# Optimization experiments

Measured on AMD Instinct MI355X. Metric: run time of the kernel, lower is better.

Reference implementation:

```python
import jax, jax.numpy as jnp
import numpy as np

D_MODEL = 1024
NUM_HEADS = 16
D_K = D_MODEL // NUM_HEADS
B, S = 4, 2048


def setup_inputs() -> dict:
    key = jax.random.key(0)
    ks = jax.random.split(key, 12)
    Q = jax.random.normal(ks[0], (B, S, D_MODEL), dtype=jnp.float32)
    K = jax.random.normal(ks[1], (B, S, D_MODEL), dtype=jnp.float32)
    V = jax.random.normal(ks[2], (B, S, D_MODEL), dtype=jnp.float32)
    # causal mask: 1 where attention allowed, 0 where blocked
    mask = jnp.tril(jnp.ones((S, S), dtype=jnp.int32))[None, None, :, :]
    sc = 1.0 / np.sqrt(D_MODEL)
    Wq = jax.random.normal(ks[3], (D_MODEL, D_MODEL), dtype=jnp.float32) * sc
    Wk = jax.random.normal(ks[4], (D_MODEL, D_MODEL), dtype=jnp.float32) * sc
    Wv = jax.random.normal(ks[5], (D_MODEL, D_MODEL), dtype=jnp.float32) * sc
    Wo = jax.random.normal(ks[6], (D_MODEL, D_MODEL), dtype=jnp.float32) * sc
    bq = jnp.zeros((D_MODEL,), dtype=jnp.float32)
    bk = jnp.zeros((D_MODEL,), dtype=jnp.float32)
    bv = jnp.zeros((D_MODEL,), dtype=jnp.float32)
    bo = jnp.zeros((D_MODEL,), dtype=jnp.float32)
    return {"Q": Q, "K": K, "V": V, "mask": mask,
            "Wq": Wq, "bq": bq, "Wk": Wk, "bk": bk,
            "Wv": Wv, "bv": bv, "Wo": Wo, "bo": bo}


def reference(Q, K, V, mask, Wq, bq, Wk, bk, Wv, bv, Wo, bo):
    b = Q.shape[0]
    # projections (torch Linear: x @ W.T + b; here W stored as [in, out])
    q = Q @ Wq + bq
    k = K @ Wk + bk
    v = V @ Wv + bv
    # [B, S, D] -> [B, H, S, d_k]
    def split_heads(x):
        return x.reshape(b, -1, NUM_HEADS, D_K).transpose(0, 2, 1, 3)
    q, k, v = split_heads(q), split_heads(k), split_heads(v)
    scores = jnp.einsum('bhqd,bhkd->bhqk', q, k) / jnp.sqrt(jnp.float32(D_K))
    scores = jnp.where(mask == 0, -jnp.inf, scores)
    attn = jax.nn.softmax(scores, axis=-1)
    out = jnp.einsum('bhqk,bhkd->bhqd', attn, v)  # [B, H, S, d_k]
    out = out.transpose(0, 2, 1, 3).reshape(b, -1, NUM_HEADS * D_K)
    return out @ Wo + bo
```

## Files before the change

### kernel.cpp

```cpp
#include <hip/hip_runtime.h>

typedef __bf16 bf16_t;
typedef __bf16 bf16x8 __attribute__((ext_vector_type(8)));
typedef __bf16 bf16x4 __attribute__((ext_vector_type(4)));
typedef float  floatx4 __attribute__((ext_vector_type(4)));

#define D_MODEL 1024
#define S_LEN   2048
#define NHEAD   16
#define DK      64
#define BATCH   4
#define MROWS   (BATCH * S_LEN)
#define QSCALE  0.18033688011112042f

__device__ __forceinline__ void load_lds16(const void* gsrc, void* ldst) {
  __builtin_amdgcn_global_load_lds(
      (const __attribute__((address_space(1))) void*)gsrc,
      (__attribute__((address_space(3))) void*)ldst, 16, 0, 0);
}

__device__ __forceinline__ unsigned pack_bf16(float a, float b) {
  union { bf16_t h[2]; unsigned u; } t;
  t.h[0] = (bf16_t)a; t.h[1] = (bf16_t)b;
  return t.u;
}

__device__ __forceinline__ float bperm_f(int addr, float v) {
  union { float f; int i; } in, out;
  in.f = v;
  out.i = __builtin_amdgcn_ds_bpermute(addr, in.i);
  return out.f;
}

__device__ __forceinline__ void barrier_mem() {
  asm volatile("" ::: "memory");
  __builtin_amdgcn_s_barrier();
  asm volatile("" ::: "memory");
}

__global__ __launch_bounds__(256)
void convert_a_kernel(const float* __restrict__ Q, const float* __restrict__ K,
                      const float* __restrict__ V, bf16_t* __restrict__ Abf)
{
  const int z = blockIdx.y;
  const float* src = z == 0 ? Q : (z == 1 ? K : V);
  bf16_t* dst = Abf + ((size_t)z << 23);
  const size_t off = ((size_t)blockIdx.x * 256 + threadIdx.x) * 8;
  floatx4 a = *(const floatx4*)&src[off];
  floatx4 b = *(const floatx4*)&src[off + 4];
  bf16x8 o;
  o[0] = (bf16_t)a[0]; o[1] = (bf16_t)a[1];
  o[2] = (bf16_t)a[2]; o[3] = (bf16_t)a[3];
  o[4] = (bf16_t)b[0]; o[5] = (bf16_t)b[1];
  o[6] = (bf16_t)b[2]; o[7] = (bf16_t)b[3];
  *(bf16x8*)&dst[off] = o;
}

__global__ __launch_bounds__(256)
void transpose_w_kernel(const float* __restrict__ W0, const float* __restrict__ W1,
                        const float* __restrict__ W2, const float* __restrict__ W3,
                        bf16_t* __restrict__ T0, bf16_t* __restrict__ T1,
                        bf16_t* __restrict__ T2, bf16_t* __restrict__ T3)
{
  const int z = blockIdx.z;
  const float* W = z == 0 ? W0 : (z == 1 ? W1 : (z == 2 ? W2 : W3));
  bf16_t* Wt     = z == 0 ? T0 : (z == 1 ? T1 : (z == 2 ? T2 : T3));

  __shared__ float tile[64][65];
  const int x0 = blockIdx.x * 64;
  const int y0 = blockIdx.y * 64;
  const int tid = threadIdx.x;
  const int r = tid >> 4;
  const int c = (tid & 15) << 2;
#pragma unroll
  for (int p = 0; p < 4; p++) {
    floatx4 v = *(const floatx4*)&W[(size_t)(y0 + p * 16 + r) * D_MODEL + x0 + c];
    tile[p * 16 + r][c + 0] = v[0];
    tile[p * 16 + r][c + 1] = v[1];
    tile[p * 16 + r][c + 2] = v[2];
    tile[p * 16 + r][c + 3] = v[3];
  }
  __syncthreads();
#pragma unroll
  for (int p = 0; p < 4; p++) {
    int row = p * 16 + r;
    bf16x4 o;
    o[0] = (bf16_t)tile[c + 0][row];
    o[1] = (bf16_t)tile[c + 1][row];
    o[2] = (bf16_t)tile[c + 2][row];
    o[3] = (bf16_t)tile[c + 3][row];
    *(bf16x4*)&Wt[(size_t)(x0 + row) * D_MODEL + y0 + c] = o;
  }
}

__global__ __launch_bounds__(512, 2)
void qkv8_kernel(const bf16_t* __restrict__ Abf, const bf16_t* __restrict__ Wcat,
                 const float* __restrict__ bq, const float* __restrict__ bk,
                 const float* __restrict__ bv,
                 bf16_t* __restrict__ qo, bf16_t* __restrict__ ko,
                 bf16_t* __restrict__ vo)
{
  __shared__ bf16_t lds[2][3][128 * 64];

  const int orig = blockIdx.x;
  const int L = (orig & 7) * 96 + (orig >> 3);
  const int bm = L / 12, bn = L % 12;
  const int m0 = bm << 7;
  const int n0 = bn << 8;
  const int z  = n0 >> 10;
  const bf16_t* A = Abf + ((size_t)z << 23);

  const int tid = threadIdx.x;
  const int wid = tid >> 6, lane = tid & 63;
  const int l15 = lane & 15, quad = lane >> 4;
  const int wm = wid >> 2, wn = wid & 3;

  floatx4 acc[4][4] = {};
  bf16x8 Af[2][2], Bf[2][2];

  auto stage_half = [&](int buf, int half, int kt) {
    const bf16_t* src = half == 0
        ? (A + (size_t)m0 * D_MODEL)
        : (Wcat + (size_t)(n0 + ((half - 1) << 7)) * D_MODEL);
    const int k0 = (kt & 15) << 6;
    bf16_t* dst = &lds[buf][half][0];
#pragma unroll
    for (int p = 0; p < 2; p++) {
      const int slot = (p << 9) + tid;
      const int row = slot >> 3;
      const int c = (slot & 7) ^ (row & 7);
      load_lds16(&src[(size_t)row * D_MODEL + k0 + (c << 3)],
                 &dst[(size_t)((p << 9) + (wid << 6)) << 3]);
    }
  };

#define PHASE(BUF, MH, NH, RDA, RDB, DOST, SBUF, SHALF, SKT, VMW)              \
  {                                                                            \
    if (RDA) {                                                                 \
      _Pragma("unroll") for (int mi = 0; mi < 2; mi++) {                       \
        const int row = (wm << 6) + (((MH) * 2 + mi) << 4) + l15;              \
        _Pragma("unroll") for (int ks = 0; ks < 2; ks++) {                     \
          const int ck = (ks << 2) + quad;                                     \
          Af[mi][ks] = *(const bf16x8*)&lds[BUF][0]                            \
              [(row << 6) + ((ck ^ (row & 7)) << 3)];                          \
        }                                                                      \
      }                                                                        \
    }                                                                          \
    if (RDB) {                                                                 \
      _Pragma("unroll") for (int ni = 0; ni < 2; ni++) {                       \
        const int row = ((wn & 1) << 6) + (((NH) * 2 + ni) << 4) + l15;        \
        _Pragma("unroll") for (int ks = 0; ks < 2; ks++) {                     \
          const int ck = (ks << 2) + quad;                                     \
          Bf[ni][ks] = *(const bf16x8*)&lds[BUF][1 + (wn >> 1)]                \
              [(row << 6) + ((ck ^ (row & 7)) << 3)];                          \
        }                                                                      \
      }                                                                        \
    }                                                                          \
    if (DOST) stage_half(SBUF, SHALF, SKT);                                    \
    barrier_mem();                                                             \
    __builtin_amdgcn_s_setprio(1);                                             \
    _Pragma("unroll") for (int mi = 0; mi < 2; mi++)                           \
      _Pragma("unroll") for (int ni = 0; ni < 2; ni++)                         \
        _Pragma("unroll") for (int ks = 0; ks < 2; ks++)                       \
          acc[(MH) * 2 + mi][(NH) * 2 + ni] =                                  \
              __builtin_amdgcn_mfma_f32_16x16x32_bf16(                         \
                  Af[mi][ks], Bf[ni][ks],                                      \
                  acc[(MH) * 2 + mi][(NH) * 2 + ni], 0, 0, 0);                 \
    __builtin_amdgcn_s_setprio(0);                                             \
    if (VMW) asm volatile("s_waitcnt vmcnt(2)" ::: "memory");                  \
    barrier_mem();                                                             \
  }

  stage_half(0, 0, 0);
  stage_half(0, 1, 0);
  stage_half(0, 2, 0);
  stage_half(1, 0, 1);
  asm volatile("s_waitcnt vmcnt(2)" ::: "memory");
  barrier_mem();

  for (int it = 0; it < 8; it++) {
    const int tv  = 2 * it + 1;
    const int tu2 = 2 * it + 2;
    const int tv2 = 2 * it + 3;
    PHASE(0, 0, 0, 1, 1, 1, 1, 1, tv,  0)
    PHASE(0, 0, 1, 0, 1, 1, 1, 2, tv,  0)
    PHASE(0, 1, 1, 1, 0, 0, 0, 0, 0,   0)
    PHASE(0, 1, 0, 0, 1, 1, 0, 0, tu2, 1)
    PHASE(1, 0, 0, 1, 1, 1, 0, 1, tu2, 0)
    PHASE(1, 0, 1, 0, 1, 1, 0, 2, tu2, 0)
    PHASE(1, 1, 1, 1, 0, 0, 0, 0, 0,   0)
    PHASE(1, 1, 0, 0, 1, 1, 1, 0, tv2, 1)
  }
  asm volatile("s_waitcnt vmcnt(0)" ::: "memory");

#undef PHASE

  const float* bias = z == 0 ? bq : (z == 1 ? bk : bv);
  bf16_t* outp      = z == 0 ? qo : (z == 1 ? ko : vo);
  const float scl   = (z == 0) ? QSCALE : 1.0f;
#pragma unroll
  for (int mi = 0; mi < 4; mi++) {
#pragma unroll
    for (int ni = 0; ni < 4; ni++) {
      const int nn = (n0 + (wn << 6) + (ni << 4) + l15) & (D_MODEL - 1);
      const float bvv = bias[nn];
      const int h = nn >> 6, d = nn & 63;
#pragma unroll
      for (int r = 0; r < 4; r++) {
        const int m = m0 + (wm << 6) + (mi << 4) + quad * 4 + r;
        const int b = m >> 11, srow = m & (S_LEN - 1);
        float v = (acc[mi][ni][r] + bvv) * scl;
        if (z < 2) {
          outp[((((size_t)(b * NHEAD + h) << 11) + srow) << 6) + d] = (bf16_t)v;
        } else {
          outp[((((size_t)(b * NHEAD + h) << 6) + d) << 11) + srow] = (bf16_t)v;
        }
      }
    }
  }
}

__global__ __launch_bounds__(256, 3)
void qkv_legacy_kernel(const float* __restrict__ Qi, const float* __restrict__ Ki,
                       const float* __restrict__ Vi, const bf16_t* __restrict__ Wcat,
                       const float* __restrict__ bq, const float* __restrict__ bk,
                       const float* __restrict__ bv,
                       bf16_t* __restrict__ qo, bf16_t* __restrict__ ko,
                       bf16_t* __restrict__ vo)
{
  __shared__ float  Asf[128 * 32];
  __shared__ bf16_t Bs[128 * 32];

  const int L = blockIdx.x + 24 * blockIdx.y;
  const int j = (L >> 3) & 7;
  const int s = ((L >> 6) << 3) | (L & 7);
  const int z = s >> 6;
  const int n0g = (((z << 3) | j)) << 7;
  const int m0 = (s & 63) << 7;

  const float* A = z == 0 ? Qi : (z == 1 ? Ki : Vi);

  const int tid = threadIdx.x;
  const int lane = tid & 63;
  const int w = tid >> 6;
  const int l15 = lane & 15;
  const int quad = lane >> 4;
  const int wy = (w >> 1) << 6;
  const int wx = (w & 1) << 6;
  const int w64 = w << 6;

  floatx4 acc[4][4];
#pragma unroll
  for (int i = 0; i < 4; i++)
#pragma unroll
    for (int jj = 0; jj < 4; jj++)
#pragma unroll
      for (int r = 0; r < 4; r++) acc[i][jj][r] = 0.0f;

  for (int kt = 0; kt < 32; kt++) {
    const int k0 = kt << 5;
    __syncthreads();
#pragma unroll
    for (int p = 0; p < 2; p++) {
      int slot = p * 256 + w64 + lane;
      int row = slot >> 2;
      int kc = (slot & 3) ^ (row & 3);
      load_lds16(&Wcat[(size_t)(n0g + row) * D_MODEL + k0 + (kc << 3)],
                 &Bs[(size_t)(p * 256 + w64) << 3]);
    }
#pragma unroll
    for (int p = 0; p < 4; p++) {
      int sbase = (w << 8) + (p << 6);
      int slot = sbase + lane;
      int row = slot >> 3;
      int ca = (slot & 7) ^ (row & 7);
      load_lds16(&A[(size_t)(m0 + row) * D_MODEL + k0 + (ca << 2)],
                 &Asf[(size_t)sbase << 2]);
    }
    __syncthreads();

    bf16x8 af[4], bfv[4];
#pragma unroll
    for (int mi = 0; mi < 4; mi++) {
      const int m = wy + mi * 16 + l15;
      const int e = m & 7;
      floatx4 f0 = *(const floatx4*)&Asf[(m << 5) + ((((quad << 1))     ^ e) << 2)];
      floatx4 f1 = *(const floatx4*)&Asf[(m << 5) + ((((quad << 1) | 1) ^ e) << 2)];
      bf16x8 o;
      o[0] = (bf16_t)f0[0]; o[1] = (bf16_t)f0[1];
      o[2] = (bf16_t)f0[2]; o[3] = (bf16_t)f0[3];
      o[4] = (bf16_t)f1[0]; o[5] = (bf16_t)f1[1];
      o[6] = (bf16_t)f1[2]; o[7] = (bf16_t)f1[3];
      af[mi] = o;
    }
#pragma unroll
    for (int ni = 0; ni < 4; ni++) {
      int n = wx + ni * 16 + l15;
      bfv[ni] = *(const bf16x8*)&Bs[n * 32 + ((quad ^ (n & 3)) << 3)];
    }
#pragma unroll
    for (int mi = 0; mi < 4; mi++)
#pragma unroll
      for (int ni = 0; ni < 4; ni++)
        acc[mi][ni] = __builtin_amdgcn_mfma_f32_16x16x32_bf16(
            af[mi], bfv[ni], acc[mi][ni], 0, 0, 0);
  }

  const float* bias = z == 0 ? bq : (z == 1 ? bk : bv);
  bf16_t* outp      = z == 0 ? qo : (z == 1 ? ko : vo);
  const float scl   = (z == 0) ? QSCALE : 1.0f;
#pragma unroll
  for (int mi = 0; mi < 4; mi++) {
#pragma unroll
    for (int ni = 0; ni < 4; ni++) {
      const int nn = (n0g + wx + ni * 16 + l15) & (D_MODEL - 1);
      const float bvv = bias[nn];
      const int h = nn >> 6, d = nn & 63;
#pragma unroll
      for (int r = 0; r < 4; r++) {
        const int m = m0 + wy + mi * 16 + quad * 4 + r;
        const int b = m >> 11, srow = m & (S_LEN - 1);
        float v = (acc[mi][ni][r] + bvv) * scl;
        if (z < 2) {
          outp[((((size_t)(b * NHEAD + h) << 11) + srow) << 6) + d] = (bf16_t)v;
        } else {
          outp[((((size_t)(b * NHEAD + h) << 6) + d) << 11) + srow] = (bf16_t)v;
        }
      }
    }
  }
}

__global__ __launch_bounds__(256)
void out_gemm_kernel(const bf16_t* __restrict__ A, const bf16_t* __restrict__ Wt,
                     const float* __restrict__ bias, float* __restrict__ out)
{
  __shared__ bf16_t As[128 * 32];
  __shared__ bf16_t Bs[128 * 32];
  const int L = blockIdx.x + 8 * blockIdx.y;
  const int n0 = (((L >> 3) & 7)) << 7;
  const int m0 = ((((L >> 6) << 3) | (L & 7))) << 7;
  const int tid = threadIdx.x;
  const int lane = tid & 63;
  const int w = tid >> 6;
  const int l15 = lane & 15;
  const int quad = lane >> 4;
  const int wy = (w >> 1) << 6;
  const int wx = (w & 1) << 6;
  const int w64 = w << 6;

  floatx4 acc[4][4];
#pragma unroll
  for (int i = 0; i < 4; i++)
#pragma unroll
    for (int jj = 0; jj < 4; jj++)
#pragma unroll
      for (int r = 0; r < 4; r++) acc[i][jj][r] = 0.0f;

  for (int kt = 0; kt < 32; kt++) {
    const int k0 = kt << 5;
    __syncthreads();
#pragma unroll
    for (int p = 0; p < 2; p++) {
      int slot = p * 256 + w64 + lane;
      int row = slot >> 2;
      int kc = (slot & 3) ^ (row & 3);
      load_lds16(&A[(size_t)(m0 + row) * D_MODEL + k0 + (kc << 3)],
                 &As[(size_t)(p * 256 + w64) << 3]);
      load_lds16(&Wt[(size_t)(n0 + row) * D_MODEL + k0 + (kc << 3)],
                 &Bs[(size_t)(p * 256 + w64) << 3]);
    }
    __syncthreads();

    bf16x8 af[4], bfv[4];
#pragma unroll
    for (int mi = 0; mi < 4; mi++) {
      int m = wy + mi * 16 + l15;
      af[mi] = *(const bf16x8*)&As[m * 32 + ((quad ^ (m & 3)) << 3)];
    }
#pragma unroll
    for (int ni = 0; ni < 4; ni++) {
      int n = wx + ni * 16 + l15;
      bfv[ni] = *(const bf16x8*)&Bs[n * 32 + ((quad ^ (n & 3)) << 3)];
    }
#pragma unroll
    for (int mi = 0; mi < 4; mi++)
#pragma unroll
      for (int ni = 0; ni < 4; ni++)
        acc[mi][ni] = __builtin_amdgcn_mfma_f32_16x16x32_bf16(
            af[mi], bfv[ni], acc[mi][ni], 0, 0, 0);
  }

#pragma unroll
  for (int mi = 0; mi < 4; mi++) {
#pragma unroll
    for (int ni = 0; ni < 4; ni++) {
      const int nbase = n0 + wx + ni * 16 + l15;
      const float bv = bias[nbase];
#pragma unroll
      for (int r = 0; r < 4; r++) {
        const int m = m0 + wy + mi * 16 + quad * 4 + r;
        out[((size_t)m << 10) + nbase] = acc[mi][ni][r] + bv;
      }
    }
  }
}

__global__ __launch_bounds__(256, 4)
void attn_kernel(const bf16_t* __restrict__ qp, const bf16_t* __restrict__ kp,
                 const bf16_t* __restrict__ vtp, bf16_t* __restrict__ ob)
{
  __shared__ bf16_t Kt0[64 * 64];
  __shared__ bf16_t Kt1[64 * 64];
  __shared__ bf16_t Vt0[64 * 64];
  __shared__ bf16_t Vt1[64 * 64];

  const int lin = blockIdx.x + (blockIdx.y << 4);
  const int pair = (lin >> 3) & 15;
  const int bh = (lin & 7) | ((lin >> 7) << 3);
  const int tid = threadIdx.x;
  const int w = tid >> 6;
  const int lane = tid & 63;
  const int l15 = lane & 15;
  const int quad = lane >> 4;

  const bf16_t* Qh = qp + ((size_t)bh << 17);
  const bf16_t* Kh = kp + ((size_t)bh << 17);
  const bf16_t* Vh = vtp + ((size_t)bh << 17);
  const int b = bh >> 4, h = bh & 15;

  auto stage = [&](int k0s, bf16_t* dK, bf16_t* dV) {
#pragma unroll
    for (int p = 0; p < 2; p++) {
      const int sbase = (w << 7) + (p << 6);
      const int slot = sbase + lane;
      const int row = slot >> 3;
      const int c = (slot & 7) ^ (row & 7);
      load_lds16(&Kh[((size_t)(k0s + row) << 6) + (c << 3)], &dK[sbase << 3]);
      load_lds16(&Vh[((size_t)row << 11) + k0s + (c << 3)], &dV[sbase << 3]);
    }
  };

  int par = 0;

  auto phase = [&](int qt, bool prefetch_next_phase) {
    const int q0 = qt << 6;
    const int qbase = q0 + (w << 4);
    const int nkb = qt + 1;

    bf16x8 qf[2];
#pragma unroll
    for (int ks = 0; ks < 2; ks++)
      qf[ks] = *(const bf16x8*)&Qh[(size_t)(qbase + l15) * DK +
                                   ks * 32 + (quad << 3)];

    floatx4 acc_o[4];
    float m_i = -1e30f, l_i = 0.0f;
#pragma unroll
    for (int nd = 0; nd < 4; nd++)
#pragma unroll
      for (int r = 0; r < 4; r++) acc_o[nd][r] = 0.0f;

    for (int kb = 0; kb < nkb; kb++) {
      const int k0 = kb << 6;
      __syncthreads();

      const bf16_t* cK = par ? Kt1 : Kt0;
      const bf16_t* cV = par ? Vt1 : Vt0;
      bf16_t* nK = par ? Kt0 : Kt1;
      bf16_t* nV = par ? Vt0 : Vt1;

      if (kb + 1 < nkb)             stage((kb + 1) << 6, nK, nV);
      else if (prefetch_next_phase) stage(0, nK, nV);

      bf16x8 bk[2][4];
#pragma unroll
      for (int ks = 0; ks < 2; ks++)
#pragma unroll
        for (int ni = 0; ni < 4; ni++) {
          const int row = ni * 16 + l15;
          const int cp = ((ks << 2) + quad) ^ (row & 7);
          bk[ks][ni] = *(const bf16x8*)&cK[(row << 6) + (cp << 3)];
        }

      floatx4 st[4];
#pragma unroll
      for (int ni = 0; ni < 4; ni++)
#pragma unroll
        for (int r = 0; r < 4; r++) st[ni][r] = 0.0f;
      __builtin_amdgcn_s_setprio(1);
#pragma unroll
      for (int ks = 0; ks < 2; ks++)
#pragma unroll
        for (int ni = 0; ni < 4; ni++)
          st[ni] = __builtin_amdgcn_mfma_f32_16x16x32_bf16(
              bk[ks][ni], qf[ks], st[ni], 0, 0, 0);
      __builtin_amdgcn_s_setprio(0);

      if (k0 + 63 > qbase) {
        const int qrow = qbase + l15;
#pragma unroll
        for (int ni = 0; ni < 4; ni++) {
          const int keyb = k0 + ni * 16 + quad * 4;
#pragma unroll
          for (int r = 0; r < 4; r++)
            if (keyb + r > qrow) st[ni][r] = -1e30f;
        }
      }

      float v = st[0][0];
#pragma unroll
      for (int ni = 0; ni < 4; ni++)
#pragma unroll
        for (int r = 0; r < 4; r++) v = fmaxf(v, st[ni][r]);
      v = fmaxf(v, __shfl_xor(v, 16));
      v = fmaxf(v, __shfl_xor(v, 32));

      if (!__all(v <= m_i + 5.0f)) {
        const float mn = fmaxf(m_i, v);
        const float alpha = __builtin_amdgcn_exp2f(m_i - mn);
        m_i = mn;
        l_i *= alpha;
#pragma unroll
        for (int r = 0; r < 4; r++) {
          float ab = bperm_f((quad * 4 + r) << 2, alpha);
#pragma unroll
          for (int nd = 0; nd < 4; nd++) acc_o[nd][r] *= ab;
        }
      }

      unsigned pd[4][2];
      float ssum = 0.0f;
#pragma unroll
      for (int c = 0; c < 4; c++)
#pragma unroll
        for (int hh = 0; hh < 2; hh++) {
          float p0 = __builtin_amdgcn_exp2f(st[c][2 * hh]     - m_i);
          float p1 = __builtin_amdgcn_exp2f(st[c][2 * hh + 1] - m_i);
          ssum += p0 + p1;
          pd[c][hh] = pack_bf16(p0, p1);
        }
      ssum += __shfl_xor(ssum, 16);
      ssum += __shfl_xor(ssum, 32);
      l_i += ssum;

      union AV { unsigned u[4]; bf16x8 v; };
      AV av[2];
#pragma unroll
      for (int ks = 0; ks < 2; ks++)
#pragma unroll
        for (int i = 0; i < 4; i++) {
          const int addr = ((((2 * quad + (i >> 1)) & 3) << 4) | l15) << 2;
          int lo = __builtin_amdgcn_ds_bpermute(addr, (int)pd[ks * 2][i & 1]);
          int hi = __builtin_amdgcn_ds_bpermute(addr, (int)pd[ks * 2 + 1][i & 1]);
          av[ks].u[i] = (unsigned)(quad >= 2 ? hi : lo);
        }

#pragma unroll
      for (int ks = 0; ks < 2; ks++) {
        bf16x8 bvv[4];
#pragma unroll
        for (int nd = 0; nd < 4; nd++) {
          const int row = nd * 16 + l15;
          const int cp = ((ks << 2) + quad) ^ (row & 7);
          bvv[nd] = *(const bf16x8*)&cV[(row << 6) + (cp << 3)];
        }
        __builtin_amdgcn_s_setprio(1);
#pragma unroll
        for (int nd = 0; nd < 4; nd++)
          acc_o[nd] = __builtin_amdgcn_mfma_f32_16x16x32_bf16(
              av[ks].v, bvv[nd], acc_o[nd], 0, 0, 0);
        __builtin_amdgcn_s_setprio(0);
      }

      par ^= 1;
    }

    const float inv = 1.0f / l_i;
#pragma unroll
    for (int r = 0; r < 4; r++) {
      const float linv = bperm_f((quad * 4 + r) << 2, inv);
      const int sRow = qbase + quad * 4 + r;
#pragma unroll
      for (int nd = 0; nd < 4; nd++) {
        const int d = nd * 16 + l15;
        ob[(((size_t)(b * S_LEN + sRow)) << 10) + h * 64 + d] =
            (bf16_t)(acc_o[nd][r] * linv);
      }
    }
  };

  stage(0, Kt0, Vt0);
  phase(31 - pair, true);
  phase(pair, false);
}

extern "C" void kernel_launch(void* const* d_in, const int* in_sizes, int n_in,
                              void* d_out, int out_size, void* d_ws, size_t ws_size,
                              hipStream_t stream)
{
  (void)in_sizes; (void)n_in; (void)out_size;
  const float* Q  = (const float*)d_in[0];
  const float* K  = (const float*)d_in[1];
  const float* V  = (const float*)d_in[2];
  const float* Wq = (const float*)d_in[4];
  const float* bq = (const float*)d_in[5];
  const float* Wk = (const float*)d_in[6];
  const float* bk = (const float*)d_in[7];
  const float* Wv = (const float*)d_in[8];
  const float* bv = (const float*)d_in[9];
  const float* Wo = (const float*)d_in[10];
  const float* bo = (const float*)d_in[11];
  float* out = (float*)d_out;

  const size_t NELT = (size_t)MROWS * D_MODEL;
  const size_t WELT = (size_t)D_MODEL * D_MODEL;

  const size_t need_new = (3 * NELT + 4 * WELT + 3 * NELT) * sizeof(bf16_t);

  bf16_t* qp   = (bf16_t*)d_ws;
  bf16_t* kp   = qp + NELT;
  bf16_t* vtp  = kp + NELT;
  bf16_t* wqt  = vtp + NELT;
  bf16_t* wkt  = wqt + WELT;
  bf16_t* wvt  = wkt + WELT;
  bf16_t* wot  = wvt + WELT;
  bf16_t* abf  = wot + WELT;
  bf16_t* obuf = abf;

  dim3 blk(256);
  transpose_w_kernel<<<dim3(16, 16, 4), blk, 0, stream>>>(
      Wq, Wk, Wv, Wo, wqt, wkt, wvt, wot);

  if (ws_size >= need_new) {
    convert_a_kernel<<<dim3(MROWS * D_MODEL / (256 * 8), 3), blk, 0, stream>>>(
        Q, K, V, abf);
    qkv8_kernel<<<dim3((MROWS / 128) * (3 * D_MODEL / 256)), dim3(512), 0,
                  stream>>>(abf, wqt, bq, bk, bv, qp, kp, vtp);
  } else {
    qkv_legacy_kernel<<<dim3(3 * D_MODEL / 128, MROWS / 128), blk, 0, stream>>>(
        Q, K, V, wqt, bq, bk, bv, qp, kp, vtp);
  }

  attn_kernel<<<dim3(16, BATCH * NHEAD), blk, 0, stream>>>(qp, kp, vtp, obuf);

  out_gemm_kernel<<<dim3(D_MODEL / 128, MROWS / 128), blk, 0, stream>>>(
      obuf, wot, bo, out);
}
```

Before: 361.4 us.

## Restructure QKV GEMM pipeline to load all fragments per buffer and prefetch deeper

The QKV projection GEMM main loop now reads all A and B fragments for a K-tile from LDS once at the start of each buffer's phases, instead of interleaving smaller reads across phases. Staging is reordered so a whole K-tile is issued ahead, with the prologue prefetching two full tiles, a wait threshold of 6 outstanding loads, and a peeled epilogue instead of wrapping the K index. The aim is fewer LDS-read stalls between MFMA groups and more in-flight global loads. The cost is more fragment registers, which may lower occupancy or cause spills.

```diff
diff --git a/kernel.cpp b/kernel.cpp
--- a/kernel.cpp
+++ b/kernel.cpp
@@ -116,13 +116,13 @@
   const int wm = wid >> 2, wn = wid & 3;
 
   floatx4 acc[4][4] = {};
-  bf16x8 Af[2][2], Bf[2][2];
+  bf16x8 Af[4][2], Bf[4][2];
 
   auto stage_half = [&](int buf, int half, int kt) {
     const bf16_t* src = half == 0
         ? (A + (size_t)m0 * D_MODEL)
         : (Wcat + (size_t)(n0 + ((half - 1) << 7)) * D_MODEL);
-    const int k0 = (kt & 15) << 6;
+    const int k0 = kt << 6;
     bf16_t* dst = &lds[buf][half][0];
 #pragma unroll
     for (int p = 0; p < 2; p++) {
@@ -134,21 +134,19 @@
     }
   };
 
-#define PHASE(BUF, MH, NH, RDA, RDB, DOST, SBUF, SHALF, SKT, VMW)              \
+#define PHASE(BUF, MH, NH, DORD, DOST, SBUF, SHALF, SKT, VMW)                  \
   {                                                                            \
-    if (RDA) {                                                                 \
-      _Pragma("unroll") for (int mi = 0; mi < 2; mi++) {                       \
-        const int row = (wm << 6) + (((MH) * 2 + mi) << 4) + l15;              \
+    if (DORD) {                                                                \
+      _Pragma("unroll") for (int mi = 0; mi < 4; mi++) {                       \
+        const int row = (wm << 6) + (mi << 4) + l15;                           \
         _Pragma("unroll") for (int ks = 0; ks < 2; ks++) {                     \
           const int ck = (ks << 2) + quad;                                     \
           Af[mi][ks] = *(const bf16x8*)&lds[BUF][0]                            \
               [(row << 6) + ((ck ^ (row & 7)) << 3)];                          \
         }                                                                      \
       }                                                                        \
-    }                                                                          \
-    if (RDB) {                                                                 \
-      _Pragma("unroll") for (int ni = 0; ni < 2; ni++) {                       \
-        const int row = ((wn & 1) << 6) + (((NH) * 2 + ni) << 4) + l15;        \
+      _Pragma("unroll") for (int ni = 0; ni < 4; ni++) {                       \
+        const int row = ((wn & 1) << 6) + (ni << 4) + l15;                     \
         _Pragma("unroll") for (int ks = 0; ks < 2; ks++) {                     \
           const int ck = (ks << 2) + quad;                                     \
           Bf[ni][ks] = *(const bf16x8*)&lds[BUF][1 + (wn >> 1)]                \
@@ -164,34 +162,43 @@
         _Pragma("unroll") for (int ks = 0; ks < 2; ks++)                       \
           acc[(MH) * 2 + mi][(NH) * 2 + ni] =                                  \
               __builtin_amdgcn_mfma_f32_16x16x32_bf16(                         \
-                  Af[mi][ks], Bf[ni][ks],                                      \
+                  Af[(MH) * 2 + mi][ks], Bf[(NH) * 2 + ni][ks],                \
                   acc[(MH) * 2 + mi][(NH) * 2 + ni], 0, 0, 0);                 \
     __builtin_amdgcn_s_setprio(0);                                             \
-    if (VMW) asm volatile("s_waitcnt vmcnt(2)" ::: "memory");                  \
+    if ((VMW) == 1) asm volatile("s_waitcnt vmcnt(6)" ::: "memory");           \
+    if ((VMW) == 2) asm volatile("s_waitcnt vmcnt(0)" ::: "memory");           \
     barrier_mem();                                                             \
   }
 
-  stage_half(0, 0, 0);
   stage_half(0, 1, 0);
   stage_half(0, 2, 0);
+  stage_half(0, 0, 0);
+  stage_half(1, 1, 1);
+  stage_half(1, 2, 1);
   stage_half(1, 0, 1);
-  asm volatile("s_waitcnt vmcnt(2)" ::: "memory");
+  asm volatile("s_waitcnt vmcnt(6)" ::: "memory");
   barrier_mem();
 
-  for (int it = 0; it < 8; it++) {
-    const int tv  = 2 * it + 1;
+  for (int it = 0; it < 7; it++) {
     const int tu2 = 2 * it + 2;
     const int tv2 = 2 * it + 3;
-    PHASE(0, 0, 0, 1, 1, 1, 1, 1, tv,  0)
-    PHASE(0, 0, 1, 0, 1, 1, 1, 2, tv,  0)
-    PHASE(0, 1, 1, 1, 0, 0, 0, 0, 0,   0)
-    PHASE(0, 1, 0, 0, 1, 1, 0, 0, tu2, 1)
-    PHASE(1, 0, 0, 1, 1, 1, 0, 1, tu2, 0)
-    PHASE(1, 0, 1, 0, 1, 1, 0, 2, tu2, 0)
-    PHASE(1, 1, 1, 1, 0, 0, 0, 0, 0,   0)
-    PHASE(1, 1, 0, 0, 1, 1, 1, 0, tv2, 1)
-  }
-  asm volatile("s_waitcnt vmcnt(0)" ::: "memory");
+    PHASE(0, 0, 0, 1, 0, 0, 0, 0,   0)
+    PHASE(0, 0, 1, 0, 1, 0, 1, tu2, 0)
+    PHASE(0, 1, 1, 0, 1, 0, 2, tu2, 0)
+    PHASE(0, 1, 0, 0, 1, 0, 0, tu2, 1)
+    PHASE(1, 0, 0, 1, 0, 0, 0, 0,   0)
+    PHASE(1, 0, 1, 0, 1, 1, 1, tv2, 0)
+    PHASE(1, 1, 1, 0, 1, 1, 2, tv2, 0)
+    PHASE(1, 1, 0, 0, 1, 1, 0, tv2, 1)
+  }
+  PHASE(0, 0, 0, 1, 0, 0, 0, 0, 0)
+  PHASE(0, 0, 1, 0, 0, 0, 0, 0, 0)
+  PHASE(0, 1, 1, 0, 0, 0, 0, 0, 0)
+  PHASE(0, 1, 0, 0, 0, 0, 0, 0, 2)
+  PHASE(1, 0, 0, 1, 0, 0, 0, 0, 0)
+  PHASE(1, 0, 1, 0, 0, 0, 0, 0, 0)
+  PHASE(1, 1, 1, 0, 0, 0, 0, 0, 0)
+  PHASE(1, 1, 0, 0, 0, 0, 0, 0, 0)
 
 #undef PHASE
 
```

Measured after the change: 356.8 us. Within noise of the previous version (-1.3%).

## Replace pipelined 8-wave QKV GEMM with simple single-buffered 128x128 kernel

Applied to the files above, without the earlier changes.

Swaps the 512-thread, 128x256-tile, double-buffered, phase-interleaved QKV projection GEMM for a 256-thread 128x128-tile kernel. The new kernel loads a K=32 slice per iteration into a single LDS buffer, with a barrier before and after each load. It also uses a different block-index swizzle for L2 locality. This removes the software pipelining and priority tricks in exchange for simpler code and smaller LDS use, but global loads no longer overlap with MFMA work.

```diff
diff --git a/kernel.cpp b/kernel.cpp
--- a/kernel.cpp
+++ b/kernel.cpp
@@ -30,12 +30,6 @@
   in.f = v;
   out.i = __builtin_amdgcn_ds_bpermute(addr, in.i);
   return out.f;
-}
-
-__device__ __forceinline__ void barrier_mem() {
-  asm volatile("" ::: "memory");
-  __builtin_amdgcn_s_barrier();
-  asm volatile("" ::: "memory");
 }
 
 __global__ __launch_bounds__(256)
@@ -93,107 +87,75 @@
   }
 }
 
-__global__ __launch_bounds__(512, 2)
-void qkv8_kernel(const bf16_t* __restrict__ Abf, const bf16_t* __restrict__ Wcat,
-                 const float* __restrict__ bq, const float* __restrict__ bk,
-                 const float* __restrict__ bv,
-                 bf16_t* __restrict__ qo, bf16_t* __restrict__ ko,
-                 bf16_t* __restrict__ vo)
+__global__ __launch_bounds__(256)
+void qkv_bf16_kernel(const bf16_t* __restrict__ Abf, const bf16_t* __restrict__ Wcat,
+                     const float* __restrict__ bq, const float* __restrict__ bk,
+                     const float* __restrict__ bv,
+                     bf16_t* __restrict__ qo, bf16_t* __restrict__ ko,
+                     bf16_t* __restrict__ vo)
 {
-  __shared__ bf16_t lds[2][3][128 * 64];
-
-  const int orig = blockIdx.x;
-  const int L = (orig & 7) * 96 + (orig >> 3);
-  const int bm = L / 12, bn = L % 12;
-  const int m0 = bm << 7;
-  const int n0 = bn << 8;
-  const int z  = n0 >> 10;
+  __shared__ bf16_t As[128 * 32];
+  __shared__ bf16_t Bs[128 * 32];
+
+  const int L = blockIdx.x + 24 * blockIdx.y;
+  const int j = (L >> 3) & 7;
+  const int s = ((L >> 6) << 3) | (L & 7);
+  const int z = s >> 6;
+  const int n0g = (((z << 3) | j)) << 7;
+  const int m0 = (s & 63) << 7;
+
   const bf16_t* A = Abf + ((size_t)z << 23);
 
   const int tid = threadIdx.x;
-  const int wid = tid >> 6, lane = tid & 63;
-  const int l15 = lane & 15, quad = lane >> 4;
-  const int wm = wid >> 2, wn = wid & 3;
-
-  floatx4 acc[4][4] = {};
-  bf16x8 Af[2][2], Bf[2][2];
-
-  auto stage_half = [&](int buf, int half, int kt) {
-    const bf16_t* src = half == 0
-        ? (A + (size_t)m0 * D_MODEL)
-        : (Wcat + (size_t)(n0 + ((half - 1) << 7)) * D_MODEL);
-    const int k0 = (kt & 15) << 6;
-    bf16_t* dst = &lds[buf][half][0];
+  const int lane = tid & 63;
+  const int w = tid >> 6;
+  const int l15 = lane & 15;
+  const int quad = lane >> 4;
+  const int wy = (w >> 1) << 6;
+  const int wx = (w & 1) << 6;
+  const int w64 = w << 6;
+
+  floatx4 acc[4][4];
+#pragma unroll
+  for (int i = 0; i < 4; i++)
+#pragma unroll
+    for (int jj = 0; jj < 4; jj++)
+#pragma unroll
+      for (int r = 0; r < 4; r++) acc[i][jj][r] = 0.0f;
+
+  for (int kt = 0; kt < 32; kt++) {
+    const int k0 = kt << 5;
+    __syncthreads();
 #pragma unroll
     for (int p = 0; p < 2; p++) {
-      const int slot = (p << 9) + tid;
-      const int row = slot >> 3;
-      const int c = (slot & 7) ^ (row & 7);
-      load_lds16(&src[(size_t)row * D_MODEL + k0 + (c << 3)],
-                 &dst[(size_t)((p << 9) + (wid << 6)) << 3]);
-    }
-  };
-
-#define PHASE(BUF, MH, NH, RDA, RDB, DOST, SBUF, SHALF, SKT, VMW)              \
-  {                                                                            \
-    if (RDA) {                                                                 \
-      _Pragma("unroll") for (int mi = 0; mi < 2; mi++) {                       \
-        const int row = (wm << 6) + (((MH) * 2 + mi) << 4) + l15;              \
-        _Pragma("unroll") for (int ks = 0; ks < 2; ks++) {                     \
-          const int ck = (ks << 2) + quad;                                     \
-          Af[mi][ks] = *(const bf16x8*)&lds[BUF][0]                            \
-              [(row << 6) + ((ck ^ (row & 7)) << 3)];                          \
-        }                                                                      \
-      }                                                                        \
-    }                                                                          \
-    if (RDB) {                                                                 \
-      _Pragma("unroll") for (int ni = 0; ni < 2; ni++) {                       \
-        const int row = ((wn & 1) << 6) + (((NH) * 2 + ni) << 4) + l15;        \
-        _Pragma("unroll") for (int ks = 0; ks < 2; ks++) {                     \
-          const int ck = (ks << 2) + quad;                                     \
-          Bf[ni][ks] = *(const bf16x8*)&lds[BUF][1 + (wn >> 1)]                \
-              [(row << 6) + ((ck ^ (row & 7)) << 3)];                          \
-        }                                                                      \
-      }                                                                        \
-    }                                                                          \
-    if (DOST) stage_half(SBUF, SHALF, SKT);                                    \
-    barrier_mem();                                                             \
-    __builtin_amdgcn_s_setprio(1);                                             \
-    _Pragma("unroll") for (int mi = 0; mi < 2; mi++)                           \
-      _Pragma("unroll") for (int ni = 0; ni < 2; ni++)                         \
-        _Pragma("unroll") for (int ks = 0; ks < 2; ks++)                       \
-          acc[(MH) * 2 + mi][(NH) * 2 + ni] =                                  \
-              __builtin_amdgcn_mfma_f32_16x16x32_bf16(                         \
-                  Af[mi][ks], Bf[ni][ks],                                      \
-                  acc[(MH) * 2 + mi][(NH) * 2 + ni], 0, 0, 0);                 \
-    __builtin_amdgcn_s_setprio(0);                                             \
-    if (VMW) asm volatile("s_waitcnt vmcnt(2)" ::: "memory");                  \
-    barrier_mem();                                                             \
-  }
-
-  stage_half(0, 0, 0);
-  stage_half(0, 1, 0);
-  stage_half(0, 2, 0);
-  stage_half(1, 0, 1);
-  asm volatile("s_waitcnt vmcnt(2)" ::: "memory");
-  barrier_mem();
-
-  for (int it = 0; it < 8; it++) {
-    const int tv  = 2 * it + 1;
-    const int tu2 = 2 * it + 2;
-    const int tv2 = 2 * it + 3;
-    PHASE(0, 0, 0, 1, 1, 1, 1, 1, tv,  0)
-    PHASE(0, 0, 1, 0, 1, 1, 1, 2, tv,  0)
-    PHASE(0, 1, 1, 1, 0, 0, 0, 0, 0,   0)
-    PHASE(0, 1, 0, 0, 1, 1, 0, 0, tu2, 1)
-    PHASE(1, 0, 0, 1, 1, 1, 0, 1, tu2, 0)
-    PHASE(1, 0, 1, 0, 1, 1, 0, 2, tu2, 0)
-    PHASE(1, 1, 1, 1, 0, 0, 0, 0, 0,   0)
-    PHASE(1, 1, 0, 0, 1, 1, 1, 0, tv2, 1)
-  }
-  asm volatile("s_waitcnt vmcnt(0)" ::: "memory");
-
-#undef PHASE
+      int slot = p * 256 + w64 + lane;
+      int row = slot >> 2;
+      int kc = (slot & 3) ^ (row & 3);
+      load_lds16(&A[(size_t)(m0 + row) * D_MODEL + k0 + (kc << 3)],
+                 &As[(size_t)(p * 256 + w64) << 3]);
+      load_lds16(&Wcat[(size_t)(n0g + row) * D_MODEL + k0 + (kc << 3)],
+                 &Bs[(size_t)(p * 256 + w64) << 3]);
+    }
+    __syncthreads();
+
+    bf16x8 af[4], bfv[4];
+#pragma unroll
+    for (int mi = 0; mi < 4; mi++) {
+      int m = wy + mi * 16 + l15;
+      af[mi] = *(const bf16x8*)&As[m * 32 + ((quad ^ (m & 3)) << 3)];
+    }
+#pragma unroll
+    for (int ni = 0; ni < 4; ni++) {
+      int n = wx + ni * 16 + l15;
+      bfv[ni] = *(const bf16x8*)&Bs[n * 32 + ((quad ^ (n & 3)) << 3)];
+    }
+#pragma unroll
+    for (int mi = 0; mi < 4; mi++)
+#pragma unroll
+      for (int ni = 0; ni < 4; ni++)
+        acc[mi][ni] = __builtin_amdgcn_mfma_f32_16x16x32_bf16(
+            af[mi], bfv[ni], acc[mi][ni], 0, 0, 0);
+  }
 
   const float* bias = z == 0 ? bq : (z == 1 ? bk : bv);
   bf16_t* outp      = z == 0 ? qo : (z == 1 ? ko : vo);
@@ -202,12 +164,12 @@
   for (int mi = 0; mi < 4; mi++) {
 #pragma unroll
     for (int ni = 0; ni < 4; ni++) {
-      const int nn = (n0 + (wn << 6) + (ni << 4) + l15) & (D_MODEL - 1);
+      const int nn = (n0g + wx + ni * 16 + l15) & (D_MODEL - 1);
       const float bvv = bias[nn];
       const int h = nn >> 6, d = nn & 63;
 #pragma unroll
       for (int r = 0; r < 4; r++) {
-        const int m = m0 + (wm << 6) + (mi << 4) + quad * 4 + r;
+        const int m = m0 + wy + mi * 16 + quad * 4 + r;
         const int b = m >> 11, srow = m & (S_LEN - 1);
         float v = (acc[mi][ni][r] + bvv) * scl;
         if (z < 2) {
@@ -635,8 +597,8 @@
   if (ws_size >= need_new) {
     convert_a_kernel<<<dim3(MROWS * D_MODEL / (256 * 8), 3), blk, 0, stream>>>(
         Q, K, V, abf);
-    qkv8_kernel<<<dim3((MROWS / 128) * (3 * D_MODEL / 256)), dim3(512), 0,
-                  stream>>>(abf, wqt, bq, bk, bv, qp, kp, vtp);
+    qkv_bf16_kernel<<<dim3(3 * D_MODEL / 128, MROWS / 128), blk, 0, stream>>>(
+        abf, wqt, bq, bk, bv, qp, kp, vtp);
   } else {
     qkv_legacy_kernel<<<dim3(3 * D_MODEL / 128, MROWS / 128), blk, 0, stream>>>(
         Q, K, V, wqt, bq, bk, bv, qp, kp, vtp);
```

New measurement: 352.2 us. 2.5% less time.
